# Optimization experiments

Hardware: AMD Instinct MI355X
Metric: run time of the kernel (lower is better)

The kernel has to match this reference:

```python
import jax, jax.numpy as jnp
import numpy as np

B, S = 16, 512
VD, TD, H, NH = 768, 768, 1024, 16
HD = H // NH
MAXREL = 128
THRESH = 2.0 / 3.0


def _bitlinear(x, W, b):
    # BitNet b1.58 eval-mode: ternary-quantize weights, rescale, dense matmul
    s = jnp.clip(jnp.mean(jnp.abs(W)), 1e-5, 1000.0)
    wn = jnp.clip(W / s, -10.0, 10.0)
    q = jnp.where(wn > THRESH, 1.0, jnp.where(wn < -THRESH, -1.0, 0.0))
    return x @ (q * s).T + b


def _ln(x, g, b, eps=1e-5):
    m = jnp.mean(x, axis=-1, keepdims=True)
    v = jnp.mean((x - m) ** 2, axis=-1, keepdims=True)
    return (x - m) * jax.lax.rsqrt(v + eps) * g + b


def setup_inputs() -> dict:
    key = jax.random.key(0)
    ks = jax.random.split(key, 10)
    def n(k, shape, std=0.02):
        return jax.random.normal(k, shape, dtype=jnp.float32) * std
    return dict(
        vision_features=jax.random.normal(ks[0], (B, VD), dtype=jnp.float32),
        text_features=jax.random.normal(ks[1], (B, S, TD), dtype=jnp.float32),
        W_vp=n(ks[2], (H, VD)), b_vp=jnp.zeros((H,), jnp.float32),
        W_tp=n(ks[3], (H, TD)), b_tp=jnp.zeros((H,), jnp.float32),
        W_tqkv=n(ks[4], (3 * H, H)), b_tqkv=jnp.zeros((3 * H,), jnp.float32),
        W_vout=n(ks[5], (H, H)), b_vout=jnp.zeros((H,), jnp.float32),
        W_tout=n(ks[6], (H, H)), b_tout=jnp.zeros((H,), jnp.float32),
        g_tn=jnp.ones((H,), jnp.float32), be_tn=jnp.zeros((H,), jnp.float32),
        g_i2t=jnp.ones((H,), jnp.float32), be_i2t=jnp.zeros((H,), jnp.float32),
        g_t2i=jnp.ones((H,), jnp.float32), be_t2i=jnp.zeros((H,), jnp.float32),
        alpha_i2t=jnp.zeros((1,), jnp.float32),
        alpha_t2i=jnp.zeros((1,), jnp.float32),
        rel_embed=n(ks[7], (2 * MAXREL + 1, NH)),
        text_mask=jnp.ones((B, S), dtype=bool),
    )


def reference(vision_features, text_features, W_vp, b_vp, W_tp, b_tp,
              W_tqkv, b_tqkv, W_vout, b_vout, W_tout, b_tout,
              g_tn, be_tn, g_i2t, be_i2t, g_t2i, be_t2i,
              alpha_i2t, alpha_t2i, rel_embed, text_mask):
    scale = HD ** -0.5
    vision_proj = _bitlinear(vision_features, W_vp, b_vp)            # [B,H]
    text_proj = _bitlinear(text_features, W_tp, b_tp)                # [B,S,H]

    # --- text self-attention with relative-position bias ---
    qkv = _bitlinear(_ln(text_proj, g_tn, be_tn), W_tqkv, b_tqkv)    # [B,S,3H]
    qkv = qkv.reshape(B, S, 3, NH, HD).transpose(2, 0, 3, 1, 4)      # [3,B,nh,S,hd]
    q, k, v = qkv[0], qkv[1], qkv[2]
    attn = jnp.einsum('bhqd,bhkd->bhqk', q, k) * scale
    coords = jnp.arange(S)
    rel = jnp.clip(coords[:, None] - coords[None, :], -MAXREL, MAXREL) + MAXREL
    attn = attn + rel_embed[rel].transpose(2, 0, 1)[None]            # +[1,nh,S,S]
    attn = jnp.where(text_mask[:, None, None, :], attn, -1e9)
    attn = jax.nn.softmax(attn, axis=-1)
    text_self = jnp.einsum('bhqk,bhkd->bhqd', attn, v)
    text_self = text_self.transpose(0, 2, 1, 3).reshape(B, S, H)
    text_self = text_proj + text_self                                # residual

    # --- image -> text cross-attention (vision token queries text) ---
    vq = jnp.broadcast_to(vision_proj[:, None], (B, S, H))
    vq = vq.reshape(B, S, NH, HD).transpose(0, 2, 1, 3)              # [B,nh,S,hd]
    tkv = text_self.reshape(B, S, NH, HD).transpose(0, 2, 1, 3)      # [B,nh,S,hd]
    i2t = jnp.einsum('bhqd,bhkd->bhqk', vq, tkv) * scale
    i2t = jnp.where(text_mask[:, None, None, :], i2t, -1e9)
    i2t = jax.nn.softmax(i2t, axis=-1)
    i2t_out = jnp.einsum('bhqk,bhkd->bhqd', i2t, tkv)
    i2t_out = i2t_out.transpose(0, 2, 1, 3).reshape(B, S, H).mean(axis=1)
    i2t_out = _ln(i2t_out, g_i2t, be_i2t)                            # [B,H]
    fused_vision = vision_proj + alpha_i2t * _bitlinear(i2t_out, W_vout, b_vout)

    # --- text -> image cross-attention (text queries single vision token) ---
    tq = text_self.reshape(B, S, NH, HD).transpose(0, 2, 1, 3)       # [B,nh,S,hd]
    vkv = vision_proj.reshape(B, 1, NH, HD).transpose(0, 2, 1, 3)    # [B,nh,1,hd]
    t2i = jnp.einsum('bhqd,bhkd->bhqk', tq, vkv) * scale             # [B,nh,S,1]
    t2i = jax.nn.softmax(t2i, axis=-1)
    t2i_out = jnp.einsum('bhqk,bhkd->bhqd', t2i, vkv)
    t2i_out = t2i_out.transpose(0, 2, 1, 3).reshape(B, S, H)
    t2i_out = _ln(t2i_out, g_t2i, be_t2i)
    fused_text = text_self + alpha_t2i * _bitlinear(t2i_out, W_tout, b_tout)

    return fused_vision, fused_text
```

## Files before the change

### kernel.cpp

```cpp
#include <hip/hip_runtime.h>
#include <cstdint>

#define B_   16
#define S_   512
#define VD_  768
#define TD_  768
#define H_   1024
#define NH_  16
#define HD_  64
#define H3_  3072

typedef __attribute__((ext_vector_type(8))) short bf16x8;
typedef __attribute__((ext_vector_type(4))) float f32x4;

__device__ __forceinline__ float b2f(unsigned short h) {
  union { unsigned u; float f; } x; x.u = ((unsigned)h) << 16; return x.f;
}
__device__ __forceinline__ unsigned short f2b(float f) {
  union { float f; unsigned u; } x; x.f = f;
  unsigned r = x.u + 0x7fffu + ((x.u >> 16) & 1u);
  return (unsigned short)(r >> 16);
}

__device__ __forceinline__ void gload_lds16(const void* g, void* lds) {
  __builtin_amdgcn_global_load_lds(
      (const __attribute__((address_space(1))) unsigned int*)g,
      (__attribute__((address_space(3))) unsigned int*)lds, 16, 0, 0);
}
__device__ __forceinline__ void lds_wave_fence() {
  __asm__ __volatile__("s_waitcnt lgkmcnt(0)" ::: "memory");
}

__global__ __launch_bounds__(256) void k_abssum_cvt(const float* __restrict__ w0, int n0,
                                                    const float* __restrict__ w1, int n1,
                                                    const float* __restrict__ w2, int n2,
                                                    const float* __restrict__ w3, int n3,
                                                    const float* __restrict__ w4, int n4,
                                                    double* __restrict__ partials,
                                                    const float* __restrict__ cvt_in,
                                                    unsigned short* __restrict__ cvt_out,
                                                    int cvt_n4) {
  int y = blockIdx.y;
  if (y == 5) {
    for (int i = blockIdx.x * 256 + threadIdx.x; i < cvt_n4; i += 128 * 256) {
      float4 v = ((const float4*)cvt_in)[i];
      ushort4 o; o.x = f2b(v.x); o.y = f2b(v.y); o.z = f2b(v.z); o.w = f2b(v.w);
      ((ushort4*)cvt_out)[i] = o;
    }
    return;
  }
  const float* w = y == 0 ? w0 : y == 1 ? w1 : y == 2 ? w2 : y == 3 ? w3 : w4;
  int n4q = (y == 0 ? n0 : y == 1 ? n1 : y == 2 ? n2 : y == 3 ? n3 : n4) >> 2;
  double s = 0.0;
  for (int i = blockIdx.x * 256 + threadIdx.x; i < n4q; i += 128 * 256) {
    float4 v = ((const float4*)w)[i];
    s += (double)fabsf(v.x) + (double)fabsf(v.y) + (double)fabsf(v.z) + (double)fabsf(v.w);
  }
#pragma unroll
  for (int off = 32; off > 0; off >>= 1) s += __shfl_down(s, off, 64);
  __shared__ double red[4];
  if ((threadIdx.x & 63) == 0) red[threadIdx.x >> 6] = s;
  __syncthreads();
  if (threadIdx.x == 0)
    partials[y * 128 + blockIdx.x] = red[0] + red[1] + red[2] + red[3];
}

__global__ __launch_bounds__(512) void k_sumfin(const double* __restrict__ partials,
                                                double* __restrict__ sums) {
  int wave = threadIdx.x >> 6, lane = threadIdx.x & 63;
  if (wave >= 5) return;
  double s = partials[wave * 128 + lane] + partials[wave * 128 + 64 + lane];
#pragma unroll
  for (int off = 32; off > 0; off >>= 1) s += __shfl_down(s, off, 64);
  if (lane == 0) sums[wave] = s;
}

__global__ __launch_bounds__(256) void k_quant5(const float* __restrict__ w0, int n0,
                                                const float* __restrict__ w1, int n1,
                                                const float* __restrict__ w2, int n2,
                                                const float* __restrict__ w3, int n3,
                                                const float* __restrict__ w4, int n4,
                                                unsigned short* __restrict__ q0,
                                                unsigned short* __restrict__ q1,
                                                unsigned short* __restrict__ q2,
                                                unsigned short* __restrict__ q3,
                                                unsigned short* __restrict__ q4,
                                                const double* __restrict__ sum,
                                                float* __restrict__ s_out) {
  int y = blockIdx.y;
  const float* w = y == 0 ? w0 : y == 1 ? w1 : y == 2 ? w2 : y == 3 ? w3 : w4;
  unsigned short* q = y == 0 ? q0 : y == 1 ? q1 : y == 2 ? q2 : y == 3 ? q3 : q4;
  int n = y == 0 ? n0 : y == 1 ? n1 : y == 2 ? n2 : y == 3 ? n3 : n4;
  double s = fmin(fmax(sum[y] / (double)n, 1e-5), 1000.0);
  if (blockIdx.x == 0 && threadIdx.x == 0) s_out[y] = (float)s;
  int i = blockIdx.x * 256 + threadIdx.x;
  if (i < n) {
    double wn = (double)w[i] / s;
    unsigned short o = 0;
    if (wn > (2.0 / 3.0)) o = 0x3F80u;
    else if (wn < -(2.0 / 3.0)) o = 0xBF80u;
    q[i] = o;
  }
}

__global__ __launch_bounds__(256) void k_rowmat(const float* __restrict__ A,
                                                const unsigned short* __restrict__ W,
                                                const float* __restrict__ sptr,
                                                const float* __restrict__ bias,
                                                float* __restrict__ Cf,
                                                unsigned short* __restrict__ Cb,
                                                const float* __restrict__ resid,
                                                const float* __restrict__ alpha,
                                                int N, int K) {
  const int t = threadIdx.x, lane = t & 63;
  const int w_idx = blockIdx.x * 4 + (t >> 6);
  const int m = w_idx / N, n = w_idx - m * N;
  const int Kper = K >> 6;
  const float* a = A + (size_t)m * K + lane * Kper;
  const unsigned short* w = W + (size_t)n * K + lane * Kper;
  float acc = 0.f;
  for (int k = 0; k < Kper; k += 4) {
    float4 av = *(const float4*)(a + k);
    ushort4 wv = *(const ushort4*)(w + k);
    acc += av.x * b2f(wv.x) + av.y * b2f(wv.y) + av.z * b2f(wv.z) + av.w * b2f(wv.w);
  }
#pragma unroll
  for (int off = 32; off > 0; off >>= 1) acc += __shfl_down(acc, off, 64);
  if (lane == 0) {
    float v = acc * sptr[0] + bias[n];
    if (resid) v = resid[w_idx] + alpha[0] * v;
    Cf[w_idx] = v;
    if (Cb) Cb[w_idx] = f2b(v);
  }
}

__global__ __launch_bounds__(256) void k_ln(const float* __restrict__ x,
                                            const float* __restrict__ g,
                                            const float* __restrict__ be,
                                            float* __restrict__ of,
                                            unsigned short* __restrict__ ob) {
  int row = blockIdx.x, t = threadIdx.x;
  const float4* xr = (const float4*)(x + (size_t)row * H_);
  float4 v = xr[t];
  float s = v.x + v.y + v.z + v.w;
  float s2 = v.x * v.x + v.y * v.y + v.z * v.z + v.w * v.w;
#pragma unroll
  for (int off = 32; off > 0; off >>= 1) { s += __shfl_down(s, off, 64); s2 += __shfl_down(s2, off, 64); }
  __shared__ float rs[4], rs2[4];
  if ((t & 63) == 0) { rs[t >> 6] = s; rs2[t >> 6] = s2; }
  __syncthreads();
  s = rs[0] + rs[1] + rs[2] + rs[3];
  s2 = rs2[0] + rs2[1] + rs2[2] + rs2[3];
  float mean = s * (1.0f / H_);
  float var = s2 * (1.0f / H_) - mean * mean;
  float rstd = rsqrtf(var + 1e-5f);
  const float4 gv = ((const float4*)g)[t];
  const float4 bv = ((const float4*)be)[t];
  float4 o;
  o.x = (v.x - mean) * rstd * gv.x + bv.x;
  o.y = (v.y - mean) * rstd * gv.y + bv.y;
  o.z = (v.z - mean) * rstd * gv.z + bv.z;
  o.w = (v.w - mean) * rstd * gv.w + bv.w;
  if (of) ((float4*)(of + (size_t)row * H_))[t] = o;
  if (ob) {
    ushort4 ou; ou.x = f2b(o.x); ou.y = f2b(o.y); ou.z = f2b(o.z); ou.w = f2b(o.w);
    ((ushort4*)(ob + (size_t)row * H_))[t] = ou;
  }
}

template <int OUTB, int VT>
__global__ __launch_bounds__(256) void k_gemm(const unsigned short* __restrict__ A,
                                              const unsigned short* __restrict__ W,
                                              const float* __restrict__ sptr,
                                              const float* __restrict__ bias,
                                              float* __restrict__ Cf,
                                              unsigned short* __restrict__ Cb,
                                              unsigned short* __restrict__ vt,
                                              int M, int N, int K) {
  __shared__ __align__(16) unsigned short As[2][128 * 32];
  __shared__ __align__(16) unsigned short Bs[2][128 * 32];
  const int t = threadIdx.x, wave = t >> 6, lane = t & 63, quad = lane >> 4, l16 = lane & 15;
  const int bm = blockIdx.y * 128, bn = blockIdx.x * 128;
  const int wm = (wave >> 1) * 64, wn = (wave & 1) * 64;
  f32x4 acc[4][4];
#pragma unroll
  for (int i = 0; i < 4; ++i)
#pragma unroll
    for (int j = 0; j < 4; ++j) acc[i][j] = f32x4{0.f, 0.f, 0.f, 0.f};

  const int srow = lane >> 2, skc = lane & 3;
  auto stage = [&](int k0, int buf) {
#pragma unroll
    for (int c = 0; c < 2; ++c) {
      int row = (wave * 2 + c) * 16 + srow;
      gload_lds16(A + (size_t)(bm + row) * K + k0 + skc * 8, &As[buf][(wave * 2 + c) * 512]);
      gload_lds16(W + (size_t)(bn + row) * K + k0 + skc * 8, &Bs[buf][(wave * 2 + c) * 512]);
    }
  };

  stage(0, 0);
  int it = 0;
  for (int k0 = 0; k0 < K; k0 += 32, ++it) {
    const int cur = it & 1;
    __syncthreads();
    if (k0 + 32 < K) stage(k0 + 32, cur ^ 1);
    bf16x8 af[4], bfrg[4];
#pragma unroll
    for (int i = 0; i < 4; ++i)
      af[i] = *(const bf16x8*)&As[cur][(wm + i * 16 + l16) * 32 + quad * 8];
#pragma unroll
    for (int j = 0; j < 4; ++j)
      bfrg[j] = *(const bf16x8*)&Bs[cur][(wn + j * 16 + l16) * 32 + quad * 8];
#pragma unroll
    for (int i = 0; i < 4; ++i)
#pragma unroll
      for (int j = 0; j < 4; ++j)
        acc[i][j] = __builtin_amdgcn_mfma_f32_16x16x32_bf16(af[i], bfrg[j], acc[i][j], 0, 0, 0);
  }
  float s = sptr[0];

  if (VT && bn >= 2 * H_) {
    __syncthreads();
    unsigned short* T = (wave < 2) ? &As[0][wave * 1152] : &Bs[0][(wave - 2) * 1152];
    const int h = (bn + wn - 2 * H_) >> 6;
    const int b = (bm + wm) >> 9, s0 = (bm + wm) & (S_ - 1);
    const int chunk0 = lane * 2;
#pragma unroll
    for (int j = 0; j < 4; ++j) {
      int n = bn + wn + j * 16 + l16;
      float bv = bias[n];
#pragma unroll
      for (int i = 0; i < 4; ++i)
#pragma unroll
        for (int r = 0; r < 4; ++r)
          T[l16 * 72 + i * 16 + quad * 4 + r] = f2b(acc[i][j][r] * s + bv);
      lds_wave_fence();
#pragma unroll
      for (int cc = 0; cc < 2; ++cc) {
        int ch = chunk0 + cc, dr = ch >> 3, k8 = ch & 7;
        uint4 val = *(const uint4*)&T[dr * 72 + k8 * 8];
        *(uint4*)(vt + ((size_t)(b * NH_ + h) * HD_ + j * 16 + dr) * S_ + s0 + k8 * 8) = val;
      }
      lds_wave_fence();
    }
    return;
  }

#pragma unroll
  for (int j = 0; j < 4; ++j) {
    int n = bn + wn + j * 16 + l16;
    float bv = bias[n];
#pragma unroll
    for (int i = 0; i < 4; ++i) {
#pragma unroll
      for (int r = 0; r < 4; ++r) {
        int m = bm + wm + i * 16 + quad * 4 + r;
        float v = acc[i][j][r] * s + bv;
        if (OUTB) Cb[(size_t)m * N + n] = f2b(v);
        else      Cf[(size_t)m * N + n] = v;
      }
    }
  }
}

__global__ __launch_bounds__(256) void k_flash(const unsigned short* __restrict__ qkv,
                                               const unsigned short* __restrict__ vt,
                                               const float* __restrict__ tp,
                                               const float* __restrict__ rel,
                                               const float* __restrict__ trow,
                                               const float* __restrict__ a_t2i,
                                               float* __restrict__ out_text,
                                               unsigned short* __restrict__ ts_b) {
  const int qt = blockIdx.x, h = blockIdx.y, b = blockIdx.z;
  __shared__ __align__(16) unsigned short Qs[64 * 64];
  __shared__ __align__(16) unsigned short Ks[2][64 * 64];
  __shared__ __align__(16) unsigned short Vs[2][64 * 64];
  __shared__ __align__(16) unsigned short Ps[4][16 * 72];
  __shared__ float rels[257];
  const int t = threadIdx.x, wave = t >> 6, lane = t & 63, quad = lane >> 4, l16 = lane & 15;
  const int srow = lane >> 3;
  const int kcg = (lane & 7) ^ srow;

  for (int i = t; i < 257; i += 256) rels[i] = rel[i * NH_ + h];

  auto stage_kv = [&](int kt, int buf) {
#pragma unroll
    for (int c = 0; c < 2; ++c) {
      int row = (wave * 2 + c) * 8 + srow;
      gload_lds16(qkv + (size_t)(b * S_ + kt * 64 + row) * H3_ + H_ + h * HD_ + kcg * 8,
                  &Ks[buf][(wave * 2 + c) * 512]);
      gload_lds16(vt + ((size_t)(b * NH_ + h) * HD_ + row) * S_ + kt * 64 + kcg * 8,
                  &Vs[buf][(wave * 2 + c) * 512]);
    }
  };

#pragma unroll
  for (int c = 0; c < 2; ++c) {
    int row = (wave * 2 + c) * 8 + srow;
    gload_lds16(qkv + (size_t)(b * S_ + qt * 64 + row) * H3_ + h * HD_ + kcg * 8,
                &Qs[(wave * 2 + c) * 512]);
  }
  stage_kv(0, 0);

  float mrun[4], lrun[4];
  f32x4 o[4];
#pragma unroll
  for (int r = 0; r < 4; ++r) { mrun[r] = -1e30f; lrun[r] = 0.f; }
#pragma unroll
  for (int j = 0; j < 4; ++j) o[j] = f32x4{0.f, 0.f, 0.f, 0.f};

  bf16x8 aq0, aq1;
  bool qloaded = false;

  for (int kt = 0; kt < 8; ++kt) {
    const int cur = kt & 1;
    __syncthreads();
    if (kt < 7) stage_kv(kt + 1, cur ^ 1);

    if (!qloaded) {
      int R = wave * 16 + l16;
      aq0 = *(const bf16x8*)&Qs[R * 64 + ((quad ^ (R & 7)) * 8)];
      aq1 = *(const bf16x8*)&Qs[R * 64 + (((4 + quad) ^ (R & 7)) * 8)];
      qloaded = true;
    }

    float pv[4][4];
#pragma unroll
    for (int j = 0; j < 4; ++j) {
      int R = j * 16 + l16;
      bf16x8 kb0 = *(const bf16x8*)&Ks[cur][R * 64 + ((quad ^ (R & 7)) * 8)];
      bf16x8 kb1 = *(const bf16x8*)&Ks[cur][R * 64 + (((4 + quad) ^ (R & 7)) * 8)];
      f32x4 z = f32x4{0.f, 0.f, 0.f, 0.f};
      z = __builtin_amdgcn_mfma_f32_16x16x32_bf16(aq0, kb0, z, 0, 0, 0);
      z = __builtin_amdgcn_mfma_f32_16x16x32_bf16(aq1, kb1, z, 0, 0, 0);
#pragma unroll
      for (int r = 0; r < 4; ++r) {
        int qg = qt * 64 + wave * 16 + quad * 4 + r;
        int kg = kt * 64 + j * 16 + l16;
        int rix = min(max(qg - kg, -128), 128) + 128;
        pv[j][r] = z[r] * 0.125f + rels[rix];
      }
    }
#pragma unroll
    for (int r = 0; r < 4; ++r) {
      float x = fmaxf(fmaxf(pv[0][r], pv[1][r]), fmaxf(pv[2][r], pv[3][r]));
#pragma unroll
      for (int off = 1; off < 16; off <<= 1) x = fmaxf(x, __shfl_xor(x, off, 64));
      float mn = fmaxf(mrun[r], x);
      float al = __expf(mrun[r] - mn);
      mrun[r] = mn;
      lrun[r] *= al;
#pragma unroll
      for (int jd = 0; jd < 4; ++jd) o[jd][r] *= al;
      float rsum = 0.f;
#pragma unroll
      for (int j = 0; j < 4; ++j) {
        float p = __expf(pv[j][r] - mn);
        pv[j][r] = p;
        rsum += p;
      }
#pragma unroll
      for (int off = 1; off < 16; off <<= 1) rsum += __shfl_xor(rsum, off, 64);
      lrun[r] += rsum;
#pragma unroll
      for (int j = 0; j < 4; ++j)
        Ps[wave][(quad * 4 + r) * 72 + j * 16 + l16] = f2b(pv[j][r]);
    }
    lds_wave_fence();
#pragma unroll
    for (int ks = 0; ks < 2; ++ks) {
      bf16x8 ap = *(const bf16x8*)&Ps[wave][l16 * 72 + ks * 32 + quad * 8];
#pragma unroll
      for (int jd = 0; jd < 4; ++jd) {
        int R = jd * 16 + l16;
        int C = ks * 4 + quad;
        bf16x8 vb = *(const bf16x8*)&Vs[cur][R * 64 + ((C ^ (R & 7)) * 8)];
        o[jd] = __builtin_amdgcn_mfma_f32_16x16x32_bf16(ap, vb, o[jd], 0, 0, 0);
      }
    }
  }
  float a2 = a_t2i[0];
#pragma unroll
  for (int jd = 0; jd < 4; ++jd) {
#pragma unroll
    for (int r = 0; r < 4; ++r) {
      int g = b * S_ + qt * 64 + wave * 16 + quad * 4 + r;
      int col = h * HD_ + jd * 16 + l16;
      float ov = o[jd][r] / lrun[r];
      float ts = tp[(size_t)g * H_ + col] + ov;
      ts_b[(size_t)g * H_ + col] = f2b(ts);
      out_text[(size_t)g * H_ + col] = ts + a2 * trow[b * H_ + col];
    }
  }
}

__global__ __launch_bounds__(256) void k_i2t(const unsigned short* __restrict__ vp_b,
                                             const unsigned short* __restrict__ ts_b,
                                             float* __restrict__ i2t_out) {
  const int h = blockIdx.x & 15, b = blockIdx.x >> 4;
  __shared__ float sc[512];
  __shared__ float red[4];
  __shared__ float qv[64];
  __shared__ float ored[4][64];
  const int t = threadIdx.x;
  if (t < 64) qv[t] = b2f(vp_b[b * H_ + h * HD_ + t]);
  __syncthreads();
  for (int k = t; k < 512; k += 256) {
    const unsigned short* kr = ts_b + (size_t)(b * S_ + k) * H_ + h * HD_;
    float acc = 0.f;
#pragma unroll
    for (int dc = 0; dc < 8; ++dc) {
      uint4 u = *(const uint4*)(kr + dc * 8);
      const unsigned short* p = (const unsigned short*)&u;
#pragma unroll
      for (int i = 0; i < 8; ++i) acc += qv[dc * 8 + i] * b2f(p[i]);
    }
    sc[k] = acc * 0.125f;
  }
  __syncthreads();
  float m = -1e30f;
  for (int k = t; k < 512; k += 256) m = fmaxf(m, sc[k]);
#pragma unroll
  for (int off = 1; off < 64; off <<= 1) m = fmaxf(m, __shfl_xor(m, off, 64));
  if ((t & 63) == 0) red[t >> 6] = m;
  __syncthreads();
  m = fmaxf(fmaxf(red[0], red[1]), fmaxf(red[2], red[3]));
  __syncthreads();
  float ls = 0.f;
  for (int k = t; k < 512; k += 256) { float p = __expf(sc[k] - m); sc[k] = p; ls += p; }
#pragma unroll
  for (int off = 1; off < 64; off <<= 1) ls += __shfl_xor(ls, off, 64);
  if ((t & 63) == 0) red[t >> 6] = ls;
  __syncthreads();
  float tot = red[0] + red[1] + red[2] + red[3];
  const int d = t & 63, grp = t >> 6;
  float acc = 0.f;
  for (int k = grp; k < 512; k += 4)
    acc += sc[k] * b2f(ts_b[(size_t)(b * S_ + k) * H_ + h * HD_ + d]);
  ored[grp][d] = acc;
  __syncthreads();
  if (t < 64)
    i2t_out[b * H_ + h * HD_ + t] = (ored[0][t] + ored[1][t] + ored[2][t] + ored[3][t]) / tot;
}

extern "C" void kernel_launch(void* const* d_in, const int* in_sizes, int n_in,
                              void* d_out, int out_size, void* d_ws, size_t ws_size,
                              hipStream_t stream) {
  const float* vf     = (const float*)d_in[0];
  const float* tf     = (const float*)d_in[1];
  const float* W_vp   = (const float*)d_in[2];
  const float* b_vp   = (const float*)d_in[3];
  const float* W_tp   = (const float*)d_in[4];
  const float* b_tp   = (const float*)d_in[5];
  const float* W_tqkv = (const float*)d_in[6];
  const float* b_tqkv = (const float*)d_in[7];
  const float* W_vout = (const float*)d_in[8];
  const float* b_vout = (const float*)d_in[9];
  const float* W_tout = (const float*)d_in[10];
  const float* b_tout = (const float*)d_in[11];
  const float* g_tn   = (const float*)d_in[12];
  const float* be_tn  = (const float*)d_in[13];
  const float* g_i2t  = (const float*)d_in[14];
  const float* be_i2t = (const float*)d_in[15];
  const float* g_t2i  = (const float*)d_in[16];
  const float* be_t2i = (const float*)d_in[17];
  const float* a_i2t  = (const float*)d_in[18];
  const float* a_t2i  = (const float*)d_in[19];
  const float* rel    = (const float*)d_in[20];

  size_t off = 0;
  auto alloc = [&](size_t bytes) -> void* {
    void* p = (char*)d_ws + off;
    off += (bytes + 255) & ~(size_t)255;
    return p;
  };
  double* sums     = (double*)alloc(64);
  double* partials = (double*)alloc(5 * 128 * 8);
  float* scales    = (float*)alloc(64);
  unsigned short* q_vp   = (unsigned short*)alloc((size_t)H_ * VD_ * 2);
  unsigned short* q_tp   = (unsigned short*)alloc((size_t)H_ * TD_ * 2);
  unsigned short* q_tqkv = (unsigned short*)alloc((size_t)H3_ * H_ * 2);
  unsigned short* q_vout = (unsigned short*)alloc((size_t)H_ * H_ * 2);
  unsigned short* q_tout = (unsigned short*)alloc((size_t)H_ * H_ * 2);
  unsigned short* tf_b   = (unsigned short*)alloc((size_t)B_ * S_ * TD_ * 2);
  float* text_proj       = (float*)alloc((size_t)B_ * S_ * H_ * 4);
  unsigned short* ln_tp  = (unsigned short*)alloc((size_t)B_ * S_ * H_ * 2);
  unsigned short* qkv    = (unsigned short*)alloc((size_t)B_ * S_ * H3_ * 2);
  unsigned short* vt     = (unsigned short*)alloc((size_t)B_ * NH_ * HD_ * S_ * 2);
  unsigned short* ts_b   = (unsigned short*)alloc((size_t)B_ * S_ * H_ * 2);
  float* vision_proj     = (float*)alloc((size_t)B_ * H_ * 4);
  unsigned short* vp_b   = (unsigned short*)alloc((size_t)B_ * H_ * 2);
  float* ln_t2i_f        = (float*)alloc((size_t)B_ * H_ * 4);
  float* trow            = (float*)alloc((size_t)B_ * H_ * 4);
  float* i2t_out         = (float*)alloc((size_t)B_ * H_ * 4);
  float* ln_i2t_f        = (float*)alloc((size_t)B_ * H_ * 4);

  float* out_vision = (float*)d_out;
  float* out_text   = (float*)d_out + B_ * H_;

  k_abssum_cvt<<<dim3(128, 6), 256, 0, stream>>>(W_vp, H_ * VD_, W_tp, H_ * TD_,
                                                 W_tqkv, H3_ * H_, W_vout, H_ * H_,
                                                 W_tout, H_ * H_, partials,
                                                 tf, tf_b, B_ * S_ * TD_ / 4);
  k_sumfin<<<1, 512, 0, stream>>>(partials, sums);
  k_quant5<<<dim3((H3_ * H_ + 255) / 256, 5), 256, 0, stream>>>(
      W_vp, H_ * VD_, W_tp, H_ * TD_, W_tqkv, H3_ * H_, W_vout, H_ * H_, W_tout, H_ * H_,
      q_vp, q_tp, q_tqkv, q_vout, q_tout, sums, scales);

  k_rowmat<<<(B_ * H_) / 4, 256, 0, stream>>>(vf, q_vp, scales + 0, b_vp,
                                              vision_proj, vp_b, nullptr, nullptr, H_, VD_);
  k_ln<<<B_, 256, 0, stream>>>(vision_proj, g_t2i, be_t2i, ln_t2i_f, nullptr);
  k_rowmat<<<(B_ * H_) / 4, 256, 0, stream>>>(ln_t2i_f, q_tout, scales + 4, b_tout,
                                              trow, nullptr, nullptr, nullptr, H_, H_);

  k_gemm<0, 0><<<dim3(H_ / 128, (B_ * S_) / 128), 256, 0, stream>>>(
      tf_b, q_tp, scales + 1, b_tp, text_proj, nullptr, nullptr, B_ * S_, H_, TD_);
  k_ln<<<B_ * S_, 256, 0, stream>>>(text_proj, g_tn, be_tn, nullptr, ln_tp);
  k_gemm<1, 1><<<dim3(H3_ / 128, (B_ * S_) / 128), 256, 0, stream>>>(
      ln_tp, q_tqkv, scales + 2, b_tqkv, nullptr, qkv, vt, B_ * S_, H3_, H_);
  k_flash<<<dim3(S_ / 64, NH_, B_), 256, 0, stream>>>(qkv, vt, text_proj, rel, trow, a_t2i,
                                                      out_text, ts_b);
  k_i2t<<<B_ * NH_, 256, 0, stream>>>(vp_b, ts_b, i2t_out);
  k_ln<<<B_, 256, 0, stream>>>(i2t_out, g_i2t, be_i2t, ln_i2t_f, nullptr);
  k_rowmat<<<(B_ * H_) / 4, 256, 0, stream>>>(ln_i2t_f, q_vout, scales + 3, b_vout,
                                              out_vision, nullptr, vision_proj, a_i2t, H_, H_);
}
```

Baseline: 405.6 us.

## Transpose QK^T MFMA in flash kernel so softmax stats stay in-lane, use exp2

Swaps the MFMA operand order in the text self-attention kernel so each lane holds one query row. Row max and sum then need two cross-quad shuffles instead of 16-lane butterflies. Folds log2e into the scale and the relative-position table so exp2 can be used. It also skips the per-element bias lookup for tiles far enough off the diagonal that the bias is constant, and skips rescaling when the running max does not change. P is packed to bf16 with v_cvt_pk_bf16_f32, and the final per-row divide becomes a multiply by the reciprocal. The costs are extra shuffles to redistribute the rescale factors and a wave-divergent branch on the rescale.

```diff
diff --git a/kernel.cpp b/kernel.cpp
--- a/kernel.cpp
+++ b/kernel.cpp
@@ -20,6 +20,18 @@
   union { float f; unsigned u; } x; x.f = f;
   unsigned r = x.u + 0x7fffu + ((x.u >> 16) & 1u);
   return (unsigned short)(r >> 16);
+}
+__device__ __forceinline__ unsigned cvt_pk_bf16(float lo, float hi) {
+  unsigned r;
+  __asm__("v_cvt_pk_bf16_f32 %0, %1, %2" : "=v"(r) : "v"(lo), "v"(hi));
+  return r;
+}
+__device__ __forceinline__ float fexp2(float x) {
+#if __has_builtin(__builtin_amdgcn_exp2f)
+  return __builtin_amdgcn_exp2f(x);
+#else
+  return exp2f(x);
+#endif
 }
 
 __device__ __forceinline__ void gload_lds16(const void* g, void* lds) {
@@ -280,8 +292,10 @@
   const int t = threadIdx.x, wave = t >> 6, lane = t & 63, quad = lane >> 4, l16 = lane & 15;
   const int srow = lane >> 3;
   const int kcg = (lane & 7) ^ srow;
-
-  for (int i = t; i < 257; i += 256) rels[i] = rel[i * NH_ + h];
+  const float LOG2E = 1.4426950408889634f;
+  const float SC = 0.125f * LOG2E;
+
+  for (int i = t; i < 257; i += 256) rels[i] = rel[i * NH_ + h] * LOG2E;
 
   auto stage_kv = [&](int kt, int buf) {
 #pragma unroll
@@ -302,15 +316,14 @@
   }
   stage_kv(0, 0);
 
-  float mrun[4], lrun[4];
+  float mrun = -1e30f, lrun = 0.f;
   f32x4 o[4];
-#pragma unroll
-  for (int r = 0; r < 4; ++r) { mrun[r] = -1e30f; lrun[r] = 0.f; }
 #pragma unroll
   for (int j = 0; j < 4; ++j) o[j] = f32x4{0.f, 0.f, 0.f, 0.f};
 
   bf16x8 aq0, aq1;
   bool qloaded = false;
+  const int qg = qt * 64 + wave * 16 + l16;
 
   for (int kt = 0; kt < 8; ++kt) {
     const int cur = kt & 1;
@@ -324,6 +337,10 @@
       qloaded = true;
     }
 
+    const int dq = qt - kt;
+    const bool uni = (dq >= 3) || (dq <= -3);
+    const float bu = uni ? rels[dq >= 3 ? 256 : 0] : 0.f;
+
     float pv[4][4];
 #pragma unroll
     for (int j = 0; j < 4; ++j) {
@@ -331,40 +348,60 @@
       bf16x8 kb0 = *(const bf16x8*)&Ks[cur][R * 64 + ((quad ^ (R & 7)) * 8)];
       bf16x8 kb1 = *(const bf16x8*)&Ks[cur][R * 64 + (((4 + quad) ^ (R & 7)) * 8)];
       f32x4 z = f32x4{0.f, 0.f, 0.f, 0.f};
-      z = __builtin_amdgcn_mfma_f32_16x16x32_bf16(aq0, kb0, z, 0, 0, 0);
-      z = __builtin_amdgcn_mfma_f32_16x16x32_bf16(aq1, kb1, z, 0, 0, 0);
+      z = __builtin_amdgcn_mfma_f32_16x16x32_bf16(kb0, aq0, z, 0, 0, 0);
+      z = __builtin_amdgcn_mfma_f32_16x16x32_bf16(kb1, aq1, z, 0, 0, 0);
+      if (uni) {
+#pragma unroll
+        for (int r = 0; r < 4; ++r) pv[j][r] = z[r] * SC + bu;
+      } else {
+        const int kg0 = kt * 64 + j * 16 + quad * 4;
+#pragma unroll
+        for (int r = 0; r < 4; ++r) {
+          int rix = min(max(qg - kg0 - r, -128), 128) + 128;
+          pv[j][r] = z[r] * SC + rels[rix];
+        }
+      }
+    }
+    float x = pv[0][0];
+#pragma unroll
+    for (int j = 0; j < 4; ++j)
+#pragma unroll
+      for (int r = 0; r < 4; ++r) x = fmaxf(x, pv[j][r]);
+    x = fmaxf(x, __shfl_xor(x, 16, 64));
+    x = fmaxf(x, __shfl_xor(x, 32, 64));
+    if (!__all(x <= mrun)) {
+      float mn = fmaxf(mrun, x);
+      float al = fexp2(mrun - mn);
+      mrun = mn;
+      lrun *= al;
+      float al0 = __shfl(al, quad * 4 + 0, 64);
+      float al1 = __shfl(al, quad * 4 + 1, 64);
+      float al2 = __shfl(al, quad * 4 + 2, 64);
+      float al3 = __shfl(al, quad * 4 + 3, 64);
+#pragma unroll
+      for (int jd = 0; jd < 4; ++jd) {
+        o[jd][0] *= al0; o[jd][1] *= al1; o[jd][2] *= al2; o[jd][3] *= al3;
+      }
+    }
+    float rsum = 0.f;
+#pragma unroll
+    for (int j = 0; j < 4; ++j)
 #pragma unroll
       for (int r = 0; r < 4; ++r) {
-        int qg = qt * 64 + wave * 16 + quad * 4 + r;
-        int kg = kt * 64 + j * 16 + l16;
-        int rix = min(max(qg - kg, -128), 128) + 128;
-        pv[j][r] = z[r] * 0.125f + rels[rix];
-      }
-    }
-#pragma unroll
-    for (int r = 0; r < 4; ++r) {
-      float x = fmaxf(fmaxf(pv[0][r], pv[1][r]), fmaxf(pv[2][r], pv[3][r]));
-#pragma unroll
-      for (int off = 1; off < 16; off <<= 1) x = fmaxf(x, __shfl_xor(x, off, 64));
-      float mn = fmaxf(mrun[r], x);
-      float al = __expf(mrun[r] - mn);
-      mrun[r] = mn;
-      lrun[r] *= al;
-#pragma unroll
-      for (int jd = 0; jd < 4; ++jd) o[jd][r] *= al;
-      float rsum = 0.f;
-#pragma unroll
-      for (int j = 0; j < 4; ++j) {
-        float p = __expf(pv[j][r] - mn);
+        float p = fexp2(pv[j][r] - mrun);
         pv[j][r] = p;
         rsum += p;
       }
-#pragma unroll
-      for (int off = 1; off < 16; off <<= 1) rsum += __shfl_xor(rsum, off, 64);
-      lrun[r] += rsum;
-#pragma unroll
-      for (int j = 0; j < 4; ++j)
-        Ps[wave][(quad * 4 + r) * 72 + j * 16 + l16] = f2b(pv[j][r]);
+    rsum += __shfl_xor(rsum, 16, 64);
+    rsum += __shfl_xor(rsum, 32, 64);
+    lrun += rsum;
+    unsigned char* psb = (unsigned char*)&Ps[wave][0] + l16 * 144 + quad * 8;
+#pragma unroll
+    for (int j = 0; j < 4; ++j) {
+      uint2 pk;
+      pk.x = cvt_pk_bf16(pv[j][0], pv[j][1]);
+      pk.y = cvt_pk_bf16(pv[j][2], pv[j][3]);
+      *(uint2*)(psb + j * 32) = pk;
     }
     lds_wave_fence();
 #pragma unroll
@@ -380,13 +417,19 @@
     }
   }
   float a2 = a_t2i[0];
+  float il[4];
+#pragma unroll
+  for (int r = 0; r < 4; ++r) {
+    float lr = __shfl(lrun, quad * 4 + r, 64);
+    il[r] = 1.0f / lr;
+  }
 #pragma unroll
   for (int jd = 0; jd < 4; ++jd) {
 #pragma unroll
     for (int r = 0; r < 4; ++r) {
       int g = b * S_ + qt * 64 + wave * 16 + quad * 4 + r;
       int col = h * HD_ + jd * 16 + l16;
-      float ov = o[jd][r] / lrun[r];
+      float ov = o[jd][r] * il[r];
       float ts = tp[(size_t)g * H_ + col] + ov;
       ts_b[(size_t)g * H_ + col] = f2b(ts);
       out_text[(size_t)g * H_ + col] = ts + a2 * trow[b * H_ + col];
```

Measured after the change: 392.8 us. 1.03x faster.
